# Kernel tuning notes

Measured on AMD Instinct MI355X. Metric: run time of the kernel, lower is better.

Reference implementation:

```python
import jax, jax.numpy as jnp
import numpy as np

N_NODES, N_EDGES, N_GRAPHS = 500000, 2000000, 16384


def _lin(key, fan_in, fan_out):
    # torch nn.Linear default init: U(-1/sqrt(fan_in), 1/sqrt(fan_in))
    s = 1.0 / np.sqrt(fan_in)
    kw, kb = jax.random.split(key)
    W = jax.random.uniform(kw, (fan_in, fan_out), jnp.float32, -s, s)
    b = jax.random.uniform(kb, (fan_out,), jnp.float32, -s, s)
    return W, b


def setup_inputs() -> dict:
    key = jax.random.key(0)
    ks = jax.random.split(key, 16)
    x = jax.random.normal(ks[0], (N_NODES, 131), jnp.float32)
    edge_src = jax.random.randint(ks[1], (N_EDGES,), 0, N_NODES, jnp.int32)
    edge_dst = jax.random.randint(ks[2], (N_EDGES,), 0, N_NODES, jnp.int32)
    batch_index = jnp.sort(jax.random.randint(ks[3], (N_NODES,), 0, N_GRAPHS, jnp.int32))
    solvent_descriptors = jax.random.normal(ks[4], (N_GRAPHS, 11), jnp.float32)
    Wc1, bc1 = _lin(ks[5], 131, 128)
    Wc2, bc2 = _lin(ks[6], 128, 64)
    W1, b1 = _lin(ks[7], 64 + 11, 2048)
    W2, b2 = _lin(ks[8], 2048, 1024)
    W3, b3 = _lin(ks[9], 1024, 128)
    # 6 property heads, stacked: Linear(128,32) -> ReLU -> Linear(32,1)
    Wh1 = jnp.stack([_lin(jax.random.fold_in(ks[10], i), 128, 32)[0] for i in range(6)])
    bh1 = jnp.stack([_lin(jax.random.fold_in(ks[10], i), 128, 32)[1] for i in range(6)])
    Wh2 = jnp.stack([_lin(jax.random.fold_in(ks[11], i), 32, 1)[0] for i in range(6)])
    bh2 = jnp.stack([_lin(jax.random.fold_in(ks[11], i), 32, 1)[1] for i in range(6)])
    return dict(x=x, edge_src=edge_src, edge_dst=edge_dst, batch_index=batch_index,
                solvent_descriptors=solvent_descriptors,
                Wc1=Wc1, bc1=bc1, Wc2=Wc2, bc2=bc2,
                W1=W1, b1=b1, W2=W2, b2=b2, W3=W3, b3=b3,
                Wh1=Wh1, bh1=bh1, Wh2=Wh2, bh2=bh2,
                num_graphs=N_GRAPHS)


def _gcn_conv(x, W, b, src, dst, n_nodes):
    # PyG GCNConv: add self-loops, symmetric normalization, scatter-add aggregate.
    h = x @ W                                           # [N, F_out]
    deg = jnp.zeros((n_nodes,), x.dtype).at[dst].add(1.0) + 1.0  # +1 for self-loop
    dinv = jax.lax.rsqrt(deg)                            # deg >= 1
    norm = dinv[src] * dinv[dst]                         # [E]
    agg = jnp.zeros_like(h).at[dst].add(norm[:, None] * h[src])
    agg = agg + h * (dinv * dinv)[:, None]               # self-loop contribution
    return agg + b


def reference(x, edge_src, edge_dst, batch_index, solvent_descriptors,
              Wc1, bc1, Wc2, bc2, W1, b1, W2, b2, W3, b3,
              Wh1, bh1, Wh2, bh2, num_graphs):
    n = x.shape[0]
    h = jax.nn.relu(_gcn_conv(x, Wc1, bc1, edge_src, edge_dst, n))
    h = _gcn_conv(h, Wc2, bc2, edge_src, edge_dst, n)
    g = jax.ops.segment_sum(h, batch_index, num_segments=num_graphs)  # global sum pool [G,64]
    z = jnp.concatenate([g, solvent_descriptors], axis=1)             # [G,75]
    z = jax.nn.relu(z @ W1 + b1)   # dropout is identity in eval
    z = jax.nn.relu(z @ W2 + b2)
    z = jax.nn.relu(z @ W3 + b3)   # [G,128]
    a = jax.nn.relu(jnp.einsum('gf,hfk->ghk', z, Wh1) + bh1)          # [G,6,32]
    out = jnp.einsum('ghk,hk->gh', a, Wh2[..., 0]) + bh2[:, 0]        # [G,6]
    return out
```

## Files before the change

kernel.cpp:

```cpp
#include <hip/hip_runtime.h>

#define N_NODES 500000
#define N_EDGES 2000000
#define N_GRAPHS 16384
#define STRIP 16
#define MPAD 500096
#define KC1 192

#define SCAN_ELEMS 2048
#define SCAN_NBLK ((N_NODES + SCAN_ELEMS - 1) / SCAN_ELEMS)

typedef short bf16x8 __attribute__((ext_vector_type(8)));
typedef float f32x4 __attribute__((ext_vector_type(4)));
typedef unsigned short u16x8 __attribute__((ext_vector_type(8)));

__device__ __forceinline__ unsigned short f2bf_rne(float x) {
    unsigned int b = __float_as_uint(x);
    unsigned int r = (b + 0x7fffu + ((b >> 16) & 1u)) >> 16;
    return (unsigned short)r;
}
__device__ __forceinline__ float bf2f(unsigned short h) {
    return __uint_as_float(((unsigned int)h) << 16);
}
__device__ __forceinline__ void split_bf(float v, unsigned short& hi, unsigned short& lo) {
    hi = f2bf_rne(v);
    lo = f2bf_rne(v - bf2f(hi));
}

__global__ __launch_bounds__(256) void k_zero_counts(int* counts) {
    int i = blockIdx.x * 256 + threadIdx.x;
    if (i < N_NODES) counts[i] = 0;
}
__global__ __launch_bounds__(256) void k_hist(const int* __restrict__ dst, int* __restrict__ counts) {
    int e = blockIdx.x * 256 + threadIdx.x;
    if (e < N_EDGES) atomicAdd(&counts[dst[e]], 1);
}
__global__ __launch_bounds__(256) void k_scan_reduce(const int* __restrict__ counts, int* __restrict__ bsum) {
    int b = blockIdx.x, t = threadIdx.x;
    int base_i = b * SCAN_ELEMS + t * 8;
    int s = 0;
    #pragma unroll
    for (int j = 0; j < 8; j++) { int i = base_i + j; if (i < N_NODES) s += counts[i]; }
    __shared__ int sh[256];
    sh[t] = s; __syncthreads();
    for (int off = 128; off > 0; off >>= 1) { if (t < off) sh[t] += sh[t + off]; __syncthreads(); }
    if (t == 0) bsum[b] = sh[0];
}
__global__ __launch_bounds__(256) void k_scan_bsum(const int* __restrict__ bsum, int* __restrict__ boff,
                                                   int* __restrict__ row_ptr) {
    __shared__ int sh[256];
    int t = threadIdx.x;
    int v = (t < SCAN_NBLK) ? bsum[t] : 0;
    sh[t] = v; __syncthreads();
    for (int off = 1; off < 256; off <<= 1) {
        int u = (t >= off) ? sh[t - off] : 0;
        __syncthreads();
        sh[t] += u; __syncthreads();
    }
    boff[t] = sh[t] - v;
    if (t == 255) row_ptr[N_NODES] = sh[255];
}
__global__ __launch_bounds__(256) void k_scan_final(const int* __restrict__ counts, const int* __restrict__ boff,
                                                    int* __restrict__ row_ptr, int* __restrict__ cursor,
                                                    float* __restrict__ dinv) {
    __shared__ int sh[256];
    int b = blockIdx.x, t = threadIdx.x;
    int base_i = b * SCAN_ELEMS + t * 8;
    int c[8]; int tsum = 0;
    #pragma unroll
    for (int j = 0; j < 8; j++) {
        int i = base_i + j;
        c[j] = (i < N_NODES) ? counts[i] : 0;
        tsum += c[j];
    }
    sh[t] = tsum; __syncthreads();
    for (int off = 1; off < 256; off <<= 1) {
        int u = (t >= off) ? sh[t - off] : 0;
        __syncthreads();
        sh[t] += u; __syncthreads();
    }
    int run = boff[b] + sh[t] - tsum;
    #pragma unroll
    for (int j = 0; j < 8; j++) {
        int i = base_i + j;
        if (i < N_NODES) {
            row_ptr[i] = run;
            cursor[i]  = run;
            dinv[i]    = rsqrtf((float)c[j] + 1.0f);
        }
        run += c[j];
    }
}
__global__ __launch_bounds__(256) void k_fill(const int* __restrict__ esrc, const int* __restrict__ edst,
                                              int* __restrict__ cursor, int* __restrict__ srcs) {
    int e = blockIdx.x * 256 + threadIdx.x;
    if (e >= N_EDGES) return;
    int d = edst[e];
    int pos = atomicAdd(&cursor[d], 1);
    srcs[pos] = esrc[e];
}
__global__ __launch_bounds__(256) void k_gstart(const int* __restrict__ batch, int* __restrict__ gstart) {
    int g = blockIdx.x * 256 + threadIdx.x;
    if (g > N_GRAPHS) return;
    if (g == N_GRAPHS) { gstart[g] = N_NODES; return; }
    int lo = 0, hi = N_NODES;
    while (lo < hi) { int mid = (lo + hi) >> 1; if (batch[mid] < g) lo = mid + 1; else hi = mid; }
    gstart[g] = lo;
}
__global__ __launch_bounds__(256) void k_zero_P(float* P) {
    int i = blockIdx.x * 256 + threadIdx.x;
    if (i < N_GRAPHS * 128) P[i] = 0.0f;
}

__global__ __launch_bounds__(256) void k_xsplit(const float* __restrict__ x, unsigned short* __restrict__ xb) {
    int idx = blockIdx.x * 256 + threadIdx.x;
    if (idx >= MPAD * (KC1 / 8)) return;
    int n = idx / (KC1 / 8);
    int c8 = (idx % (KC1 / 8)) * 8;
    u16x8 o;
    #pragma unroll
    for (int j = 0; j < 8; j++) {
        int k = c8 + j;
        float v = (k < 131 && n < N_NODES) ? x[(size_t)n * 131 + k] : 0.0f;
        o[j] = f2bf_rne(v);
    }
    *(u16x8*)(xb + (size_t)n * KC1 + c8) = o;
}

__global__ __launch_bounds__(256) void k_wc1split(const float* __restrict__ W,
                                                  unsigned short* __restrict__ Th,
                                                  unsigned short* __restrict__ Tl) {
    int idx = blockIdx.x * 256 + threadIdx.x;
    if (idx >= 128 * KC1) return;
    int c = idx / KC1, k = idx % KC1;
    float v = (k < 131) ? W[(size_t)k * 128 + c] : 0.0f;
    unsigned short hi, lo; split_bf(v, hi, lo);
    Th[idx] = hi; Tl[idx] = lo;
}

__global__ __launch_bounds__(256) void k_mfma_conv1(const unsigned short* __restrict__ Abf,
                                                    const unsigned short* __restrict__ Bh,
                                                    const unsigned short* __restrict__ Bl,
                                                    unsigned short* __restrict__ C) {
    __shared__ short lds[24576];
    const int tid = threadIdx.x;
    const int w = tid >> 6, l = tid & 63;
    const int bm = blockIdx.x;
    const int wm = w >> 1, wn = w & 1;
    const int lane15 = l & 15, lg = l >> 4, l7 = l & 7;
    const int koffg = ((l & 7) ^ ((l >> 3) & 7)) * 8;
    f32x4 acc[4][4] = {};
    for (int kt = 0; kt < 3; kt++) {
        const int k0 = kt * 64;
        __syncthreads();
        if (w < 2) {
            #pragma unroll
            for (int i = 0; i < 8; i++) {
                size_t row = (size_t)bm * 128 + w * 64 + i * 8 + (l >> 3);
                const unsigned short* src = Abf + row * KC1 + k0 + koffg;
                __builtin_amdgcn_global_load_lds(
                    (const __attribute__((address_space(1))) unsigned int*)src,
                    (__attribute__((address_space(3))) unsigned int*)&lds[w * 4096 + i * 512],
                    16, 0, 0);
            }
        } else {
            const unsigned short* gB = (w == 2) ? Bh : Bl;
            #pragma unroll
            for (int i = 0; i < 16; i++) {
                int row = i * 8 + (l >> 3);
                const unsigned short* src = gB + (size_t)row * KC1 + k0 + koffg;
                __builtin_amdgcn_global_load_lds(
                    (const __attribute__((address_space(1))) unsigned int*)src,
                    (__attribute__((address_space(3))) unsigned int*)&lds[(w - 1) * 8192 + i * 512],
                    16, 0, 0);
            }
        }
        __syncthreads();
        #pragma unroll
        for (int kh = 0; kh < 2; kh++) {
            const int slot = ((kh * 4 + lg) ^ l7) * 8;
            bf16x8 af[4], bhf[4], blf[4];
            #pragma unroll
            for (int m = 0; m < 4; m++)
                af[m] = *(const bf16x8*)&lds[(wm * 64 + m * 16 + lane15) * 64 + slot];
            #pragma unroll
            for (int n = 0; n < 4; n++) {
                int si = (wn * 64 + n * 16 + lane15) * 64 + slot;
                bhf[n] = *(const bf16x8*)&lds[8192 + si];
                blf[n] = *(const bf16x8*)&lds[16384 + si];
            }
            #pragma unroll
            for (int m = 0; m < 4; m++)
                #pragma unroll
                for (int n = 0; n < 4; n++) {
                    acc[m][n] = __builtin_amdgcn_mfma_f32_16x16x32_bf16(af[m], bhf[n], acc[m][n], 0, 0, 0);
                    acc[m][n] = __builtin_amdgcn_mfma_f32_16x16x32_bf16(af[m], blf[n], acc[m][n], 0, 0, 0);
                }
        }
    }
    const size_t row_b = (size_t)bm * 128 + wm * 64 + lg * 4;
    const int col_b = wn * 64 + lane15;
    #pragma unroll
    for (int m = 0; m < 4; m++)
        #pragma unroll
        for (int n = 0; n < 4; n++) {
            int col = col_b + n * 16;
            #pragma unroll
            for (int j = 0; j < 4; j++) {
                size_t row = row_b + m * 16 + j;
                if (row < N_NODES)
                    C[row * 128 + col] = f2bf_rne(acc[m][n][j]);
            }
        }
}

__global__ __launch_bounds__(256) void k_gather1(const unsigned short* __restrict__ h,
                                                 const float* __restrict__ dinv,
                                                 const float* __restrict__ bias,
                                                 const int* __restrict__ row_ptr, const int* __restrict__ srcs,
                                                 unsigned short* __restrict__ r1) {
    int g = blockIdx.x * 256 + threadIdx.x;
    int n = g >> 6, lane = g & 63;
    if (n >= N_NODES) return;
    float dn = dinv[n];
    int c = lane * 2;
    unsigned int hv = *(const unsigned int*)(h + (size_t)n * 128 + c);
    float s2 = dn * dn;
    float a0 = fmaf(s2, bf2f((unsigned short)(hv & 0xffffu)), bias[c]);
    float a1 = fmaf(s2, bf2f((unsigned short)(hv >> 16)), bias[c + 1]);
    int e0 = row_ptr[n], e1 = row_ptr[n + 1];
    int e = e0;
    for (; e + 2 <= e1; e += 2) {
        int sA = srcs[e], sB = srcs[e + 1];
        float nA = dinv[sA] * dn, nB = dinv[sB] * dn;
        unsigned int hA = *(const unsigned int*)(h + (size_t)sA * 128 + c);
        unsigned int hB = *(const unsigned int*)(h + (size_t)sB * 128 + c);
        a0 = fmaf(nA, bf2f((unsigned short)(hA & 0xffffu)), a0);
        a1 = fmaf(nA, bf2f((unsigned short)(hA >> 16)), a1);
        a0 = fmaf(nB, bf2f((unsigned short)(hB & 0xffffu)), a0);
        a1 = fmaf(nB, bf2f((unsigned short)(hB >> 16)), a1);
    }
    if (e < e1) {
        int sA = srcs[e];
        float nA = dinv[sA] * dn;
        unsigned int hA = *(const unsigned int*)(h + (size_t)sA * 128 + c);
        a0 = fmaf(nA, bf2f((unsigned short)(hA & 0xffffu)), a0);
        a1 = fmaf(nA, bf2f((unsigned short)(hA >> 16)), a1);
    }
    a0 = fmaxf(a0, 0.0f);
    a1 = fmaxf(a1, 0.0f);
    unsigned int o = (unsigned int)f2bf_rne(a0) | ((unsigned int)f2bf_rne(a1) << 16);
    *(unsigned int*)(r1 + (size_t)n * 128 + c) = o;
}

__global__ __launch_bounds__(256) void k_g2p(const unsigned short* __restrict__ r1,
                                             const float* __restrict__ dinv,
                                             const int* __restrict__ row_ptr, const int* __restrict__ srcs,
                                             const int* __restrict__ batch,
                                             float* __restrict__ P) {
    int gw = (blockIdx.x * 256 + threadIdx.x) >> 6;
    int lane = threadIdx.x & 63;
    if (gw >= N_NODES / STRIP) return;
    int n0 = gw * STRIP;
    int c = lane * 2;
    float a0 = 0.0f, a1 = 0.0f;
    int cur_g = batch[n0];
    for (int n = n0; n < n0 + STRIP; n++) {
        int bg = batch[n];
        if (bg != cur_g) {
            atomicAdd(&P[(size_t)cur_g * 128 + c], a0);
            atomicAdd(&P[(size_t)cur_g * 128 + c + 1], a1);
            a0 = a1 = 0.0f;
            cur_g = bg;
        }
        float dn = dinv[n];
        float s2 = dn * dn;
        unsigned int hv = *(const unsigned int*)(r1 + (size_t)n * 128 + c);
        a0 = fmaf(s2, bf2f((unsigned short)(hv & 0xffffu)), a0);
        a1 = fmaf(s2, bf2f((unsigned short)(hv >> 16)), a1);
        int e0 = row_ptr[n], e1 = row_ptr[n + 1];
        int e = e0;
        for (; e + 2 <= e1; e += 2) {
            int sA = srcs[e], sB = srcs[e + 1];
            float nA = dinv[sA] * dn, nB = dinv[sB] * dn;
            unsigned int hA = *(const unsigned int*)(r1 + (size_t)sA * 128 + c);
            unsigned int hB = *(const unsigned int*)(r1 + (size_t)sB * 128 + c);
            a0 = fmaf(nA, bf2f((unsigned short)(hA & 0xffffu)), a0);
            a1 = fmaf(nA, bf2f((unsigned short)(hA >> 16)), a1);
            a0 = fmaf(nB, bf2f((unsigned short)(hB & 0xffffu)), a0);
            a1 = fmaf(nB, bf2f((unsigned short)(hB >> 16)), a1);
        }
        if (e < e1) {
            int sA = srcs[e];
            float nA = dinv[sA] * dn;
            unsigned int hA = *(const unsigned int*)(r1 + (size_t)sA * 128 + c);
            a0 = fmaf(nA, bf2f((unsigned short)(hA & 0xffffu)), a0);
            a1 = fmaf(nA, bf2f((unsigned short)(hA >> 16)), a1);
        }
    }
    atomicAdd(&P[(size_t)cur_g * 128 + c], a0);
    atomicAdd(&P[(size_t)cur_g * 128 + c + 1], a1);
}

__global__ __launch_bounds__(128) void k_zg(const float* __restrict__ P, const int* __restrict__ gstart,
                                            const float* __restrict__ Wc2, const float* __restrict__ bc2,
                                            const float* __restrict__ solv, float* __restrict__ zpad) {
    int g = blockIdx.x; int c = threadIdx.x;
    if (c >= 80) return;
    float v = 0.0f;
    if (c < 64) {
        const float* pr = P + (size_t)g * 128;
        float s = 0.0f;
        #pragma unroll 8
        for (int k = 0; k < 128; k++) s = fmaf(pr[k], Wc2[k * 64 + c], s);
        v = s + (float)(gstart[g + 1] - gstart[g]) * bc2[c];
    } else if (c < 75) {
        v = solv[g * 11 + (c - 64)];
    }
    zpad[(size_t)g * 80 + c] = v;
}

__global__ __launch_bounds__(256) void k_w1pad(const float* __restrict__ W1, float* __restrict__ w1pad) {
    int i = blockIdx.x * 256 + threadIdx.x;
    if (i >= 80 * 2048) return;
    int r = i / 2048, c = i % 2048;
    w1pad[i] = (r < 75) ? W1[r * 2048 + c] : 0.0f;
}

__global__ __launch_bounds__(256) void k_whcat(const float* __restrict__ Wh1, float* __restrict__ whcat) {
    int i = blockIdx.x * 256 + threadIdx.x;
    if (i >= 128 * 256) return;
    int f = i / 256, c = i % 256;
    float v = 0.0f;
    if (c < 192) {
        int h = c / 32, k = c & 31;
        v = Wh1[h * 128 * 32 + f * 32 + k];
    }
    whcat[i] = v;
}
__global__ __launch_bounds__(256) void k_bh1pad(const float* __restrict__ bh1, float* __restrict__ bh1pad) {
    int i = threadIdx.x;
    bh1pad[i] = (i < 192) ? bh1[i] : 0.0f;
}

__global__ __launch_bounds__(256) void k_tsplit(const float* __restrict__ W, int R, int C,
                                                unsigned short* __restrict__ Th, unsigned short* __restrict__ Tl) {
    __shared__ float tile[64][65];
    int cb = blockIdx.x * 64, rb = blockIdx.y * 64;
    int tc = threadIdx.x & 63, tr4 = threadIdx.x >> 6;
    #pragma unroll 4
    for (int i = 0; i < 16; i++) {
        int r = tr4 + i * 4;
        tile[r][tc] = W[(size_t)(rb + r) * C + cb + tc];
    }
    __syncthreads();
    #pragma unroll 4
    for (int i = 0; i < 16; i++) {
        int r = tr4 + i * 4;
        float v = tile[tc][r];
        unsigned short hi, lo; split_bf(v, hi, lo);
        size_t o = (size_t)(cb + r) * R + rb + tc;
        Th[o] = hi; Tl[o] = lo;
    }
}

template<bool RELU, int OMODE>
__global__ __launch_bounds__(256) void k_gemm(const float* __restrict__ A,
                                              const float* __restrict__ B,
                                              const float* __restrict__ bias,
                                              float* __restrict__ C,
                                              unsigned short* __restrict__ Ch,
                                              unsigned short* __restrict__ Cl,
                                              int M, int N, int K) {
    __shared__ float As[8][132];
    __shared__ float Bs[8][132];
    const int tid = threadIdx.x;
    const int bm = blockIdx.y, bn = blockIdx.x;
    const int tr = (tid >> 4) << 3;
    const int tc = (tid & 15) << 3;
    float acc[8][8] = {};
    const float* Ab = A + (size_t)bm * 128 * K;
    const float* Bb = B + (size_t)bn * 128;
    const int la_r = tid >> 1, la_c = (tid & 1) << 2;
    const int lb_r = tid >> 5, lb_c = (tid & 31) << 2;
    for (int k0 = 0; k0 < K; k0 += 8) {
        float4 a4 = *(const float4*)(Ab + (size_t)la_r * K + k0 + la_c);
        float4 b4 = *(const float4*)(Bb + (size_t)(k0 + lb_r) * N + lb_c);
        __syncthreads();
        As[la_c + 0][la_r] = a4.x;
        As[la_c + 1][la_r] = a4.y;
        As[la_c + 2][la_r] = a4.z;
        As[la_c + 3][la_r] = a4.w;
        *(float4*)&Bs[lb_r][lb_c] = b4;
        __syncthreads();
        #pragma unroll
        for (int k = 0; k < 8; k++) {
            float a[8], b[8];
            *(float4*)&a[0] = *(const float4*)&As[k][tr];
            *(float4*)&a[4] = *(const float4*)&As[k][tr + 4];
            *(float4*)&b[0] = *(const float4*)&Bs[k][tc];
            *(float4*)&b[4] = *(const float4*)&Bs[k][tc + 4];
            #pragma unroll
            for (int i = 0; i < 8; i++)
                #pragma unroll
                for (int j = 0; j < 8; j++)
                    acc[i][j] = fmaf(a[i], b[j], acc[i][j]);
        }
    }
    const int row0 = bm * 128 + tr, col0 = bn * 128 + tc;
    #pragma unroll
    for (int i = 0; i < 8; i++) {
        if (OMODE == 0) {
            #pragma unroll
            for (int j = 0; j < 8; j++) {
                float v = acc[i][j] + bias[col0 + j];
                if (RELU) v = fmaxf(v, 0.0f);
                acc[i][j] = v;
            }
            *(float4*)(C + (size_t)(row0 + i) * N + col0)     = *(float4*)&acc[i][0];
            *(float4*)(C + (size_t)(row0 + i) * N + col0 + 4) = *(float4*)&acc[i][4];
        } else {
            u16x8 h8, l8;
            #pragma unroll
            for (int j = 0; j < 8; j++) {
                float v = acc[i][j] + bias[col0 + j];
                if (RELU) v = fmaxf(v, 0.0f);
                unsigned short hi, lo; split_bf(v, hi, lo);
                h8[j] = hi; l8[j] = lo;
            }
            *(u16x8*)(Ch + (size_t)(row0 + i) * N + col0) = h8;
            *(u16x8*)(Cl + (size_t)(row0 + i) * N + col0) = l8;
        }
    }
}

template<int OMODE>
__global__ __launch_bounds__(256) void k_mfma_split(
        const unsigned short* __restrict__ Ah, const unsigned short* __restrict__ Al,
        const unsigned short* __restrict__ Bh, const unsigned short* __restrict__ Bl,
        const float* __restrict__ bias,
        float* __restrict__ C, unsigned short* __restrict__ Ch, unsigned short* __restrict__ Cl,
        int N, int K) {
    __shared__ short lds[32768];
    const int tid = threadIdx.x;
    const int w = tid >> 6, l = tid & 63;
    const int id = blockIdx.x;
    const int bm = id & 127;
    const int bn = id >> 7;
    const unsigned short* gmat = (w == 0) ? Ah : (w == 1) ? Al : (w == 2) ? Bh : Bl;
    const size_t grow0 = (size_t)((w < 2) ? bm : bn) * 128 + (l >> 3);
    const int koffg = ((l & 7) ^ ((l >> 3) & 7)) * 8;
    const int ldsw = w * 8192;
    const int wm = w >> 1, wn = w & 1;
    const int lane15 = l & 15, lg = l >> 4, l7 = l & 7;
    f32x4 acc[4][4] = {};
    const int NK = K >> 6;
    for (int kt = 0; kt < NK; kt++) {
        const int k0 = kt << 6;
        __syncthreads();
        #pragma unroll
        for (int i = 0; i < 16; i++) {
            const unsigned short* src = gmat + (grow0 + (size_t)i * 8) * (size_t)K + k0 + koffg;
            __builtin_amdgcn_global_load_lds(
                (const __attribute__((address_space(1))) unsigned int*)src,
                (__attribute__((address_space(3))) unsigned int*)&lds[ldsw + i * 512],
                16, 0, 0);
        }
        __syncthreads();
        #pragma unroll
        for (int kh = 0; kh < 2; kh++) {
            const int slot = ((kh * 4 + lg) ^ l7) * 8;
            bf16x8 ahf[4], alf[4], bhf[4], blf[4];
            #pragma unroll
            for (int m = 0; m < 4; m++) {
                int si = (wm * 64 + m * 16 + lane15) * 64 + slot;
                ahf[m] = *(const bf16x8*)&lds[si];
                alf[m] = *(const bf16x8*)&lds[8192 + si];
            }
            #pragma unroll
            for (int n = 0; n < 4; n++) {
                int si = (wn * 64 + n * 16 + lane15) * 64 + slot;
                bhf[n] = *(const bf16x8*)&lds[16384 + si];
                blf[n] = *(const bf16x8*)&lds[24576 + si];
            }
            #pragma unroll
            for (int m = 0; m < 4; m++)
                #pragma unroll
                for (int n = 0; n < 4; n++) {
                    acc[m][n] = __builtin_amdgcn_mfma_f32_16x16x32_bf16(ahf[m], bhf[n], acc[m][n], 0, 0, 0);
                    acc[m][n] = __builtin_amdgcn_mfma_f32_16x16x32_bf16(ahf[m], blf[n], acc[m][n], 0, 0, 0);
                    acc[m][n] = __builtin_amdgcn_mfma_f32_16x16x32_bf16(alf[m], bhf[n], acc[m][n], 0, 0, 0);
                }
        }
    }
    const int row_b = bm * 128 + wm * 64 + lg * 4;
    const int col_b = bn * 128 + wn * 64 + lane15;
    #pragma unroll
    for (int m = 0; m < 4; m++)
        #pragma unroll
        for (int n = 0; n < 4; n++) {
            int col = col_b + n * 16;
            float bv = bias[col];
            #pragma unroll
            for (int j = 0; j < 4; j++) {
                int row = row_b + m * 16 + j;
                float v = fmaxf(acc[m][n][j] + bv, 0.0f);
                size_t o = (size_t)row * N + col;
                if (OMODE == 0) {
                    C[o] = v;
                } else {
                    unsigned short hi, lo; split_bf(v, hi, lo);
                    Ch[o] = hi; Cl[o] = lo;
                }
            }
        }
}

__global__ __launch_bounds__(256) void k_heads_out(const float* __restrict__ a,
                                                   const float* __restrict__ Wh2,
                                                   const float* __restrict__ bh2,
                                                   float* __restrict__ out) {
    int i = blockIdx.x * 256 + threadIdx.x;
    if (i >= N_GRAPHS * 6) return;
    int g = i / 6, h = i % 6;
    const float* ap = a + (size_t)g * 256 + h * 32;
    const float* wp = Wh2 + h * 32;
    float s = 0.0f;
    #pragma unroll
    for (int k = 0; k < 32; k++) s = fmaf(ap[k], wp[k], s);
    out[i] = s + bh2[h];
}

extern "C" void kernel_launch(void* const* d_in, const int* in_sizes, int n_in,
                              void* d_out, int out_size, void* d_ws, size_t ws_size,
                              hipStream_t stream) {
    const float* x    = (const float*)d_in[0];
    const int*   esrc = (const int*)d_in[1];
    const int*   edst = (const int*)d_in[2];
    const int*   batch= (const int*)d_in[3];
    const float* solv = (const float*)d_in[4];
    const float* Wc1  = (const float*)d_in[5];
    const float* bc1  = (const float*)d_in[6];
    const float* Wc2  = (const float*)d_in[7];
    const float* bc2  = (const float*)d_in[8];
    const float* W1   = (const float*)d_in[9];
    const float* b1   = (const float*)d_in[10];
    const float* W2   = (const float*)d_in[11];
    const float* b2   = (const float*)d_in[12];
    const float* W3   = (const float*)d_in[13];
    const float* b3   = (const float*)d_in[14];
    const float* Wh1  = (const float*)d_in[15];
    const float* bh1  = (const float*)d_in[16];
    const float* Wh2  = (const float*)d_in[17];
    const float* bh2  = (const float*)d_in[18];
    float* out = (float*)d_out;

    float* ws    = (float*)d_ws;
    float* bufA  = ws;
    float* bufB  = bufA + 64000000;
    float* dinv  = bufB + 64000000;
    float* zpad  = dinv + 524288;
    float* w1pad = zpad + (size_t)N_GRAPHS * 80;
    float* whcat = w1pad + 80 * 2048;
    float* bh1p  = whcat + 128 * 256;
    int* counts  = (int*)(bh1p + 256);
    int* row_ptr = counts + N_NODES;
    int* cursor  = row_ptr + 500224;
    int* srcs    = cursor + N_NODES;
    int* bsum    = srcs + N_EDGES;
    int* boff    = bsum + 256;
    int* gstart  = boff + 256;
    float* P     = bufB + 61902848;

    unsigned short* h_bf = (unsigned short*)bufA;
    unsigned short* x_bf = (unsigned short*)bufB;
    unsigned short* r1   = (unsigned short*)bufB;
    unsigned short* wc1h = (unsigned short*)(bufA + 60000000);
    unsigned short* wc1l = wc1h + 128 * KC1;

    unsigned short* z1h = (unsigned short*)bufB;
    unsigned short* z1l = (unsigned short*)(bufB + 16800000);
    unsigned short* z2h = (unsigned short*)bufA;
    unsigned short* z2l = (unsigned short*)(bufA + 8400000);
    float* z3 = bufB + 34000000;
    unsigned short* w2th = (unsigned short*)(bufA + 33000000);
    unsigned short* w2tl = (unsigned short*)(bufA + 34100000);
    unsigned short* w3th = (unsigned short*)(bufA + 35200000);
    unsigned short* w3tl = (unsigned short*)(bufA + 35300000);
    float* ab = bufA + 36000000;

    k_zero_counts<<<(N_NODES + 255) / 256, 256, 0, stream>>>(counts);
    k_hist<<<(N_EDGES + 255) / 256, 256, 0, stream>>>(edst, counts);
    k_scan_reduce<<<SCAN_NBLK, 256, 0, stream>>>(counts, bsum);
    k_scan_bsum<<<1, 256, 0, stream>>>(bsum, boff, row_ptr);
    k_scan_final<<<SCAN_NBLK, 256, 0, stream>>>(counts, boff, row_ptr, cursor, dinv);
    k_fill<<<(N_EDGES + 255) / 256, 256, 0, stream>>>(esrc, edst, cursor, srcs);
    k_gstart<<<(N_GRAPHS + 256) / 256, 256, 0, stream>>>(batch, gstart);
    k_zero_P<<<(N_GRAPHS * 128) / 256, 256, 0, stream>>>(P);

    k_xsplit<<<(MPAD * (KC1 / 8) + 255) / 256, 256, 0, stream>>>(x, x_bf);
    k_wc1split<<<(128 * KC1 + 255) / 256, 256, 0, stream>>>(Wc1, wc1h, wc1l);
    k_mfma_conv1<<<MPAD / 128, 256, 0, stream>>>(x_bf, wc1h, wc1l, h_bf);

    k_gather1<<<(N_NODES * 64) / 256, 256, 0, stream>>>(h_bf, dinv, bc1, row_ptr, srcs, r1);

    k_g2p<<<((N_NODES / STRIP) * 64 + 255) / 256, 256, 0, stream>>>(r1, dinv, row_ptr, srcs, batch, P);

    k_tsplit<<<dim3(1024 / 64, 2048 / 64), 256, 0, stream>>>(W2, 2048, 1024, w2th, w2tl);
    k_tsplit<<<dim3(128 / 64, 1024 / 64), 256, 0, stream>>>(W3, 1024, 128, w3th, w3tl);

    k_zg<<<N_GRAPHS, 128, 0, stream>>>(P, gstart, Wc2, bc2, solv, zpad);

    k_w1pad<<<(80 * 2048) / 256, 256, 0, stream>>>(W1, w1pad);
    k_whcat<<<(128 * 256) / 256, 256, 0, stream>>>(Wh1, whcat);
    k_bh1pad<<<1, 256, 0, stream>>>(bh1, bh1p);

    k_gemm<true, 1><<<dim3(2048 / 128, N_GRAPHS / 128), 256, 0, stream>>>(
        zpad, w1pad, b1, nullptr, z1h, z1l, N_GRAPHS, 2048, 80);
    k_mfma_split<1><<<(1024 / 128) * (N_GRAPHS / 128), 256, 0, stream>>>(
        z1h, z1l, w2th, w2tl, b2, nullptr, z2h, z2l, 1024, 2048);
    k_mfma_split<0><<<(128 / 128) * (N_GRAPHS / 128), 256, 0, stream>>>(
        z2h, z2l, w3th, w3tl, b3, z3, nullptr, nullptr, 128, 1024);

    k_gemm<true, 0><<<dim3(256 / 128, N_GRAPHS / 128), 256, 0, stream>>>(
        z3, whcat, bh1p, ab, nullptr, nullptr, N_GRAPHS, 256, 128);
    k_heads_out<<<(N_GRAPHS * 6 + 255) / 256, 256, 0, stream>>>(ab, Wh2, bh2, out);
}
```

Baseline: 1.224 ms.

## Fuse fp32-to-bf16 conversion of x into conv1 GEMM and unroll gathers

Drops the separate pass that converted x to a padded bf16 buffer. The conv1 MFMA kernel now reads fp32 x directly, converts it in registers and writes it to LDS, which removes one full write and re-read of a roughly 190 MB intermediate. The two edge-gather kernels are unrolled from 2 to 4 edges per iteration to raise memory-level parallelism, and r1 is written with nontemporal stores. In exchange, the A-tile loads are now unaligned per-thread fp32 reads of odd-stride rows instead of async global-to-LDS copies. That may lower load efficiency inside the GEMM.

```diff
diff --git a/kernel.cpp b/kernel.cpp
--- a/kernel.cpp
+++ b/kernel.cpp
@@ -4,7 +4,6 @@
 #define N_EDGES 2000000
 #define N_GRAPHS 16384
 #define STRIP 16
-#define MPAD 500096
 #define KC1 192
 
 #define SCAN_ELEMS 2048
@@ -112,21 +111,6 @@
     if (i < N_GRAPHS * 128) P[i] = 0.0f;
 }
 
-__global__ __launch_bounds__(256) void k_xsplit(const float* __restrict__ x, unsigned short* __restrict__ xb) {
-    int idx = blockIdx.x * 256 + threadIdx.x;
-    if (idx >= MPAD * (KC1 / 8)) return;
-    int n = idx / (KC1 / 8);
-    int c8 = (idx % (KC1 / 8)) * 8;
-    u16x8 o;
-    #pragma unroll
-    for (int j = 0; j < 8; j++) {
-        int k = c8 + j;
-        float v = (k < 131 && n < N_NODES) ? x[(size_t)n * 131 + k] : 0.0f;
-        o[j] = f2bf_rne(v);
-    }
-    *(u16x8*)(xb + (size_t)n * KC1 + c8) = o;
-}
-
 __global__ __launch_bounds__(256) void k_wc1split(const float* __restrict__ W,
                                                   unsigned short* __restrict__ Th,
                                                   unsigned short* __restrict__ Tl) {
@@ -138,7 +122,7 @@
     Th[idx] = hi; Tl[idx] = lo;
 }
 
-__global__ __launch_bounds__(256) void k_mfma_conv1(const unsigned short* __restrict__ Abf,
+__global__ __launch_bounds__(256) void k_mfma_conv1(const float* __restrict__ X,
                                                     const unsigned short* __restrict__ Bh,
                                                     const unsigned short* __restrict__ Bl,
                                                     unsigned short* __restrict__ C) {
@@ -152,17 +136,30 @@
     f32x4 acc[4][4] = {};
     for (int kt = 0; kt < 3; kt++) {
         const int k0 = kt * 64;
-        __syncthreads();
+        u16x8 a_st[8];
         if (w < 2) {
             #pragma unroll
             for (int i = 0; i < 8; i++) {
-                size_t row = (size_t)bm * 128 + w * 64 + i * 8 + (l >> 3);
-                const unsigned short* src = Abf + row * KC1 + k0 + koffg;
-                __builtin_amdgcn_global_load_lds(
-                    (const __attribute__((address_space(1))) unsigned int*)src,
-                    (__attribute__((address_space(3))) unsigned int*)&lds[w * 4096 + i * 512],
-                    16, 0, 0);
-            }
+                int row = bm * 128 + w * 64 + i * 8 + (l >> 3);
+                if (row >= N_NODES) row = N_NODES - 1;
+                const float* src = X + (size_t)row * 131 + k0 + koffg;
+                if (kt < 2) {
+                    #pragma unroll
+                    for (int j = 0; j < 8; j++) a_st[i][j] = f2bf_rne(src[j]);
+                } else {
+                    #pragma unroll
+                    for (int j = 0; j < 8; j++) {
+                        int k = k0 + koffg + j;
+                        a_st[i][j] = (k < 131) ? f2bf_rne(src[j]) : (unsigned short)0;
+                    }
+                }
+            }
+        }
+        __syncthreads();
+        if (w < 2) {
+            #pragma unroll
+            for (int i = 0; i < 8; i++)
+                *(u16x8*)&lds[w * 4096 + i * 512 + l * 8] = a_st[i];
         } else {
             const unsigned short* gB = (w == 2) ? Bh : Bl;
             #pragma unroll
@@ -230,17 +227,23 @@
     float a1 = fmaf(s2, bf2f((unsigned short)(hv >> 16)), bias[c + 1]);
     int e0 = row_ptr[n], e1 = row_ptr[n + 1];
     int e = e0;
-    for (; e + 2 <= e1; e += 2) {
-        int sA = srcs[e], sB = srcs[e + 1];
-        float nA = dinv[sA] * dn, nB = dinv[sB] * dn;
+    for (; e + 4 <= e1; e += 4) {
+        int sA = srcs[e], sB = srcs[e + 1], sC = srcs[e + 2], sD = srcs[e + 3];
+        float nA = dinv[sA] * dn, nB = dinv[sB] * dn, nC = dinv[sC] * dn, nD = dinv[sD] * dn;
         unsigned int hA = *(const unsigned int*)(h + (size_t)sA * 128 + c);
         unsigned int hB = *(const unsigned int*)(h + (size_t)sB * 128 + c);
+        unsigned int hC = *(const unsigned int*)(h + (size_t)sC * 128 + c);
+        unsigned int hD = *(const unsigned int*)(h + (size_t)sD * 128 + c);
         a0 = fmaf(nA, bf2f((unsigned short)(hA & 0xffffu)), a0);
         a1 = fmaf(nA, bf2f((unsigned short)(hA >> 16)), a1);
         a0 = fmaf(nB, bf2f((unsigned short)(hB & 0xffffu)), a0);
         a1 = fmaf(nB, bf2f((unsigned short)(hB >> 16)), a1);
-    }
-    if (e < e1) {
+        a0 = fmaf(nC, bf2f((unsigned short)(hC & 0xffffu)), a0);
+        a1 = fmaf(nC, bf2f((unsigned short)(hC >> 16)), a1);
+        a0 = fmaf(nD, bf2f((unsigned short)(hD & 0xffffu)), a0);
+        a1 = fmaf(nD, bf2f((unsigned short)(hD >> 16)), a1);
+    }
+    for (; e < e1; e++) {
         int sA = srcs[e];
         float nA = dinv[sA] * dn;
         unsigned int hA = *(const unsigned int*)(h + (size_t)sA * 128 + c);
@@ -250,7 +253,7 @@
     a0 = fmaxf(a0, 0.0f);
     a1 = fmaxf(a1, 0.0f);
     unsigned int o = (unsigned int)f2bf_rne(a0) | ((unsigned int)f2bf_rne(a1) << 16);
-    *(unsigned int*)(r1 + (size_t)n * 128 + c) = o;
+    __builtin_nontemporal_store(o, (unsigned int*)(r1 + (size_t)n * 128 + c));
 }
 
 __global__ __launch_bounds__(256) void k_g2p(const unsigned short* __restrict__ r1,
@@ -280,17 +283,23 @@
         a1 = fmaf(s2, bf2f((unsigned short)(hv >> 16)), a1);
         int e0 = row_ptr[n], e1 = row_ptr[n + 1];
         int e = e0;
-        for (; e + 2 <= e1; e += 2) {
-            int sA = srcs[e], sB = srcs[e + 1];
-            float nA = dinv[sA] * dn, nB = dinv[sB] * dn;
+        for (; e + 4 <= e1; e += 4) {
+            int sA = srcs[e], sB = srcs[e + 1], sC = srcs[e + 2], sD = srcs[e + 3];
+            float nA = dinv[sA] * dn, nB = dinv[sB] * dn, nC = dinv[sC] * dn, nD = dinv[sD] * dn;
             unsigned int hA = *(const unsigned int*)(r1 + (size_t)sA * 128 + c);
             unsigned int hB = *(const unsigned int*)(r1 + (size_t)sB * 128 + c);
+            unsigned int hC = *(const unsigned int*)(r1 + (size_t)sC * 128 + c);
+            unsigned int hD = *(const unsigned int*)(r1 + (size_t)sD * 128 + c);
             a0 = fmaf(nA, bf2f((unsigned short)(hA & 0xffffu)), a0);
             a1 = fmaf(nA, bf2f((unsigned short)(hA >> 16)), a1);
             a0 = fmaf(nB, bf2f((unsigned short)(hB & 0xffffu)), a0);
             a1 = fmaf(nB, bf2f((unsigned short)(hB >> 16)), a1);
-        }
-        if (e < e1) {
+            a0 = fmaf(nC, bf2f((unsigned short)(hC & 0xffffu)), a0);
+            a1 = fmaf(nC, bf2f((unsigned short)(hC >> 16)), a1);
+            a0 = fmaf(nD, bf2f((unsigned short)(hD & 0xffffu)), a0);
+            a1 = fmaf(nD, bf2f((unsigned short)(hD >> 16)), a1);
+        }
+        for (; e < e1; e++) {
             int sA = srcs[e];
             float nA = dinv[sA] * dn;
             unsigned int hA = *(const unsigned int*)(r1 + (size_t)sA * 128 + c);
@@ -573,7 +582,6 @@
     float* P     = bufB + 61902848;
 
     unsigned short* h_bf = (unsigned short*)bufA;
-    unsigned short* x_bf = (unsigned short*)bufB;
     unsigned short* r1   = (unsigned short*)bufB;
     unsigned short* wc1h = (unsigned short*)(bufA + 60000000);
     unsigned short* wc1l = wc1h + 128 * KC1;
@@ -598,9 +606,8 @@
     k_gstart<<<(N_GRAPHS + 256) / 256, 256, 0, stream>>>(batch, gstart);
     k_zero_P<<<(N_GRAPHS * 128) / 256, 256, 0, stream>>>(P);
 
-    k_xsplit<<<(MPAD * (KC1 / 8) + 255) / 256, 256, 0, stream>>>(x, x_bf);
     k_wc1split<<<(128 * KC1 + 255) / 256, 256, 0, stream>>>(Wc1, wc1h, wc1l);
-    k_mfma_conv1<<<MPAD / 128, 256, 0, stream>>>(x_bf, wc1h, wc1l, h_bf);
+    k_mfma_conv1<<<(N_NODES + 127) / 128, 256, 0, stream>>>(x, wc1h, wc1l, h_bf);
 
     k_gather1<<<(N_NODES * 64) / 256, 256, 0, stream>>>(h_bf, dinv, bc1, row_ptr, srcs, r1);
 
```

After: 1.123 ms. 8.2% less time.
